# Optimization experiments

Measured on AMD Instinct MI355X. Metric: run time of the kernel, lower is better.

The kernel has to match this reference:

```python
import jax, jax.numpy as jnp
import numpy as np
from jax import lax

L, H, DH, D, FF = 8, 16, 64, 1024, 4096  # layers, heads, head dim, model dim, mlp hidden
B, S = 4, 512
EPS = 1e-5


def setup_inputs() -> dict:
    key = jax.random.key(0)
    ks = jax.random.split(key, 8)
    std = 0.02
    return {
        "x": jax.random.normal(ks[0], (B, S, D), jnp.float32),
        "ln1_w": jnp.ones((L, D), jnp.float32),
        "ln1_b": jnp.zeros((L, D), jnp.float32),
        "qw": jax.random.normal(ks[1], (L, H, DH, DH), jnp.float32) * std,
        "qb": jnp.zeros((L, H, DH), jnp.float32),
        "kw": jax.random.normal(ks[2], (L, H, DH, DH), jnp.float32) * std,
        "kb": jnp.zeros((L, H, DH), jnp.float32),
        "vw": jax.random.normal(ks[3], (L, H, DH, DH), jnp.float32) * std,
        "vb": jnp.zeros((L, H, DH), jnp.float32),
        "ln2_w": jnp.ones((L, D), jnp.float32),
        "ln2_b": jnp.zeros((L, D), jnp.float32),
        "w1": jax.random.normal(ks[4], (L, D, FF), jnp.float32) * std,
        "b1": jnp.zeros((L, FF), jnp.float32),
        "w2": jax.random.normal(ks[5], (L, FF, D), jnp.float32) * std,
        "b2": jnp.zeros((L, D), jnp.float32),
    }


def _layernorm(x, w, b):
    m = jnp.mean(x, axis=-1, keepdims=True)
    v = jnp.mean(jnp.square(x - m), axis=-1, keepdims=True)
    return (x - m) * lax.rsqrt(v + EPS) * w + b


def reference(x, ln1_w, ln1_b, qw, qb, kw, kb, vw, vb, ln2_w, ln2_b, w1, b1, w2, b2):
    b, s, d = x.shape
    scale = 1.0 / jnp.sqrt(jnp.asarray(DH, x.dtype))

    def layer(h, p):
        (l1w, l1b, Qw, Qb, Kw, Kb, Vw, Vb, l2w, l2b, W1, B1, W2, B2) = p
        y = _layernorm(h, l1w, l1b)
        yh = y.reshape(b, s, H, DH)
        # nn.Linear per head: y @ W.T + b, W is [out=e, in=d]
        q = jnp.einsum('bshd,hed->bshe', yh, Qw) + Qb
        k = jnp.einsum('bshd,hed->bshe', yh, Kw) + Kb
        v = jnp.einsum('bshd,hed->bshe', yh, Vw) + Vb
        attn = jax.nn.softmax(jnp.einsum('bshe,bthe->bhst', q, k) * scale, axis=-1)
        o = jnp.einsum('bhst,bthe->bshe', attn, v).reshape(b, s, d)
        h = h + o
        z = _layernorm(h, l2w, l2b)
        z = jax.nn.gelu(z @ W1 + B1, approximate=False) @ W2 + B2
        return h + z, None

    params = (ln1_w, ln1_b, qw, qb, kw, kb, vw, vb, ln2_w, ln2_b, w1, b1, w2, b2)
    out, _ = lax.scan(layer, x, params)
    return out
```

## Files before the change

kernel.cpp:

```cpp
#include <hip/hip_runtime.h>
#include <hip/hip_bf16.h>

typedef __hip_bfloat16 bf16;
typedef __bf16 bf16x8 __attribute__((ext_vector_type(8)));
typedef float f32x4 __attribute__((ext_vector_type(4)));
typedef unsigned short u16;
typedef unsigned int u32;

#define SEQ 512
#define DMODEL 1024
#define FFDIM 4096
#define NHEAD 16
#define HDIM 64
#define NB 4
#define NLAYER 8

#define SBAR() asm volatile("s_barrier" ::: "memory")

__device__ __forceinline__ u16 f2bu(float f) {
    union { bf16 h; u16 u; } c; c.h = __float2bfloat16(f); return c.u;
}

__device__ __forceinline__ void gload16(const bf16* g, bf16* l) {
    __builtin_amdgcn_global_load_lds(
        (const __attribute__((address_space(1))) unsigned int*)g,
        (__attribute__((address_space(3))) unsigned int*)l,
        16, 0, 0);
}

__device__ __forceinline__ void gemm_pipe(
    const bf16* __restrict__ A, int lda,
    const bf16* __restrict__ B, int ldb,
    int nkt,
    f32x4 (&acc)[8][2],
    char* lA, char* lB)
{
    const int tid = threadIdx.x;
    const int lane = tid & 63;
    const int wave = tid >> 6;
    const int wr = wave >> 2, wc = wave & 3;
    const int l15 = lane & 15, l4 = lane >> 4;

    auto stage = [&](int c, int t) {
        const bf16* Ak = A + t * 64;
        const bf16* Bk = B + t * 64;
        bf16* dA = (bf16*)(lA + c * 32768);
        bf16* dB = (bf16*)(lB + c * 16384);
#pragma unroll
        for (int it = 0; it < 4; ++it) {
            const int e = (it * 512 + tid) * 8;
            const int r = e >> 6;
            const int cb = (e & 63) * 2;
            const int sc = (cb ^ (((r >> 2) & 1) << 5)) >> 1;
            gload16(Ak + (long)r * lda + sc, dA + e);
        }
#pragma unroll
        for (int it = 0; it < 2; ++it) {
            const int e = (it * 512 + tid) * 8;
            const int r = e >> 6;
            const int cb = (e & 63) * 2;
            const int sc = (cb ^ (((r >> 2) & 1) << 5)) >> 1;
            gload16(Bk + (long)r * ldb + sc, dB + e);
        }
    };

    stage(0, 0);
    stage(1, 1);
    asm volatile("s_waitcnt vmcnt(6)" ::: "memory");
    SBAR();

    for (int t = 0; t < nkt; ++t) {
        const int cur = t & 1;
        const char* bA = lA + cur * 32768;
        const char* bB = lB + cur * 16384;

        bf16x8 bf_[2][2];
#pragma unroll
        for (int fn = 0; fn < 2; ++fn)
#pragma unroll
            for (int ks = 0; ks < 2; ++ks) {
                const int row = wc * 32 + fn * 16 + l15;
                int byte = row * 128 + (ks * 32 + l4 * 8) * 2;
                byte ^= ((row >> 2) & 1) << 5;
                bf_[fn][ks] = *(const bf16x8*)(bB + byte);
            }
#pragma unroll
        for (int q = 0; q < 4; ++q) {
            bf16x8 af[2][2];
#pragma unroll
            for (int i = 0; i < 2; ++i)
#pragma unroll
                for (int ks = 0; ks < 2; ++ks) {
                    const int row = wr * 128 + (q * 2 + i) * 16 + l15;
                    int byte = row * 128 + (ks * 32 + l4 * 8) * 2;
                    byte ^= ((row >> 2) & 1) << 5;
                    af[i][ks] = *(const bf16x8*)(bA + byte);
                }
            __builtin_amdgcn_s_setprio(1);
#pragma unroll
            for (int i = 0; i < 2; ++i)
#pragma unroll
                for (int fn = 0; fn < 2; ++fn)
#pragma unroll
                    for (int ks = 0; ks < 2; ++ks)
                        acc[q * 2 + i][fn] = __builtin_amdgcn_mfma_f32_16x16x32_bf16(
                            af[i][ks], bf_[fn][ks], acc[q * 2 + i][fn], 0, 0, 0);
            __builtin_amdgcn_s_setprio(0);
        }
        SBAR();
        if (t + 2 < nkt) {
            stage(cur, t + 2);
            asm volatile("s_waitcnt vmcnt(6)" ::: "memory");
        } else {
            asm volatile("s_waitcnt vmcnt(0)" ::: "memory");
        }
        SBAR();
    }
}

__global__ __launch_bounds__(256) void k_ln(const float* __restrict__ h,
                                            const float* __restrict__ w,
                                            const float* __restrict__ bp,
                                            bf16* __restrict__ out)
{
    const int row = blockIdx.x;
    const int tid = threadIdx.x;
    const float4 x = ((const float4*)(h + (long)row * DMODEL))[tid];
    float s  = x.x + x.y + x.z + x.w;
    float s2 = x.x * x.x + x.y * x.y + x.z * x.z + x.w * x.w;
#pragma unroll
    for (int off = 32; off; off >>= 1) { s += __shfl_xor(s, off); s2 += __shfl_xor(s2, off); }
    __shared__ float rs[4], rs2[4];
    const int wave = tid >> 6;
    if ((tid & 63) == 0) { rs[wave] = s; rs2[wave] = s2; }
    __syncthreads();
    const float S1 = rs[0] + rs[1] + rs[2] + rs[3];
    const float S2 = rs2[0] + rs2[1] + rs2[2] + rs2[3];
    const float mean = S1 * (1.0f / DMODEL);
    const float var  = S2 * (1.0f / DMODEL) - mean * mean;
    const float rstd = rsqrtf(var + 1e-5f);
    const float4 wv = ((const float4*)w)[tid];
    const float4 bv = ((const float4*)bp)[tid];
    uint2 o;
    o.x = (u32)f2bu((x.x - mean) * rstd * wv.x + bv.x) |
          ((u32)f2bu((x.y - mean) * rstd * wv.y + bv.y) << 16);
    o.y = (u32)f2bu((x.z - mean) * rstd * wv.z + bv.z) |
          ((u32)f2bu((x.w - mean) * rstd * wv.w + bv.w) << 16);
    ((uint2*)(out + (long)row * DMODEL))[tid] = o;
}

__global__ __launch_bounds__(256) void k_transw_all(const float* __restrict__ w1,
                                                    const float* __restrict__ w2,
                                                    bf16* __restrict__ w1t,
                                                    bf16* __restrict__ w2t)
{
    __shared__ float t[64][65];
    int bid = blockIdx.x;
    const int l = bid >> 11;
    bid &= 2047;
    const long lofs = (long)l * DMODEL * FFDIM;
    const float* src; bf16* dst; int R, C, rb, cb;
    if (bid < 1024) {
        src = w1 + lofs; dst = w1t + lofs; R = DMODEL; C = FFDIM;
        rb = (bid >> 6) << 6; cb = (bid & 63) << 6;
    } else {
        bid -= 1024;
        src = w2 + lofs; dst = w2t + lofs; R = FFDIM; C = DMODEL;
        rb = (bid >> 4) << 6; cb = (bid & 15) << 6;
    }
    const int tid = threadIdx.x;
    const int lr = tid >> 4;
    const int lc = (tid & 15) * 4;
#pragma unroll
    for (int i = 0; i < 4; ++i) {
        const int r = i * 16 + lr;
        const float4 v = *(const float4*)(src + (long)(rb + r) * C + cb + lc);
        t[r][lc] = v.x; t[r][lc + 1] = v.y; t[r][lc + 2] = v.z; t[r][lc + 3] = v.w;
    }
    __syncthreads();
#pragma unroll
    for (int i = 0; i < 4; ++i) {
        const int c = i * 16 + lr;
        uint2 o;
        o.x = (u32)f2bu(t[lc][c])     | ((u32)f2bu(t[lc + 1][c]) << 16);
        o.y = (u32)f2bu(t[lc + 2][c]) | ((u32)f2bu(t[lc + 3][c]) << 16);
        *(uint2*)(dst + (long)(cb + c) * R + rb + lc) = o;
    }
}

__global__ __launch_bounds__(256) void k_qkv2(const bf16* __restrict__ y,
                                              const float* __restrict__ qwl,
                                              const float* __restrict__ kwl,
                                              const float* __restrict__ vwl,
                                              const float* __restrict__ qb,
                                              const float* __restrict__ kb,
                                              const float* __restrict__ vb,
                                              bf16* __restrict__ qh,
                                              bf16* __restrict__ kh,
                                              bf16* __restrict__ vt)
{
    __shared__ __align__(16) char lmem[128 * 64 * 2 + 64 * 64 * 2];
    bf16* lA = (bf16*)lmem;
    char* lBb = lmem + 128 * 64 * 2;

    const int tid = threadIdx.x;
    const int lane = tid & 63, wave = tid >> 6;
    const int l15 = lane & 15, l4 = lane >> 4;
    const int z = blockIdx.y;
    const int b = z >> 4, hd = z & 15;
    const bf16* A = y + (long)b * SEQ * DMODEL + hd * HDIM + (long)blockIdx.x * 128 * DMODEL;

#pragma unroll
    for (int it = 0; it < 4; ++it) {
        const int f = (it * 256 + tid) * 8;
        const int r = f >> 6, c = f & 63;
        gload16(A + (long)r * DMODEL + c, lA + f);
    }
    __syncthreads();

    bf16x8 qa[2][2];
#pragma unroll
    for (int fm = 0; fm < 2; ++fm)
#pragma unroll
        for (int ks = 0; ks < 2; ++ks)
            qa[fm][ks] = *(const bf16x8*)(lA + (wave * 32 + fm * 16 + l15) * 64 + ks * 32 + l4 * 8);

    for (int t = 0; t < 3; ++t) {
        __syncthreads();
        const float* Bsrc = ((t == 0) ? qwl : (t == 1) ? kwl : vwl) + (long)hd * HDIM * HDIM;
#pragma unroll
        for (int it = 0; it < 4; ++it) {
            const int f = (it * 256 + tid) * 4;
            const float4 v = *(const float4*)(Bsrc + f);
            uint2 o;
            o.x = (u32)f2bu(v.x) | ((u32)f2bu(v.y) << 16);
            o.y = (u32)f2bu(v.z) | ((u32)f2bu(v.w) << 16);
            const int row = f >> 6;
            const int byte = (f << 1) ^ ((row & 7) << 4);
            *(uint2*)(lBb + byte) = o;
        }
        __syncthreads();

        bf16x8 bfr[4][2];
#pragma unroll
        for (int fn = 0; fn < 4; ++fn)
#pragma unroll
            for (int ks = 0; ks < 2; ++ks) {
                const int row = fn * 16 + l15;
                int byte = (row << 7) + ((ks * 32 + l4 * 8) << 1);
                byte ^= (row & 7) << 4;
                bfr[fn][ks] = *(const bf16x8*)(lBb + byte);
            }
        f32x4 acc[2][4] = {};
#pragma unroll
        for (int ks = 0; ks < 2; ++ks)
#pragma unroll
            for (int fm = 0; fm < 2; ++fm)
#pragma unroll
                for (int fn = 0; fn < 4; ++fn)
                    acc[fm][fn] = __builtin_amdgcn_mfma_f32_16x16x32_bf16(
                        qa[fm][ks], bfr[fn][ks], acc[fm][fn], 0, 0, 0);

        const float* bias = (t == 0) ? qb : (t == 1) ? kb : vb;
#pragma unroll
        for (int fm = 0; fm < 2; ++fm)
#pragma unroll
            for (int fn = 0; fn < 4; ++fn)
#pragma unroll
                for (int r = 0; r < 4; ++r) {
                    const int srow = blockIdx.x * 128 + wave * 32 + fm * 16 + l4 * 4 + r;
                    const int e = fn * 16 + l15;
                    float v = acc[fm][fn][r] + bias[hd * HDIM + e];
                    if (t == 0) {
                        qh[((long)z * SEQ + srow) * HDIM + e] = __float2bfloat16(v * 0.125f);
                    } else if (t == 1) {
                        kh[((long)z * SEQ + srow) * HDIM + e] = __float2bfloat16(v);
                    } else {
                        vt[((long)z * HDIM + e) * SEQ + srow] = __float2bfloat16(v);
                    }
                }
    }
}

__global__ __launch_bounds__(256) void k_flash(const bf16* __restrict__ qh,
                                               const bf16* __restrict__ kh,
                                               const bf16* __restrict__ vt,
                                               float* __restrict__ h)
{
    __shared__ __align__(16) char lmem[24576];
    bf16* lQ = (bf16*)lmem;
    char* lKb = lmem + 8192;
    char* lVb = lmem + 16384;

    const int tid = threadIdx.x;
    const int lane = tid & 63, wave = tid >> 6;
    const int l15 = lane & 15, l4 = lane >> 4;
    const int z = blockIdx.y;
    const int b = z >> 4, hd = z & 15;
    const int q0 = blockIdx.x * 64;

    const bf16* Qsrc = qh + ((long)z * SEQ + q0) * HDIM;
#pragma unroll
    for (int it = 0; it < 2; ++it) {
        const int f = (it * 256 + tid) * 8;
        gload16(Qsrc + f, lQ + f);
    }
    __syncthreads();

    bf16x8 qa[2];
#pragma unroll
    for (int ks = 0; ks < 2; ++ks)
        qa[ks] = *(const bf16x8*)(lQ + (wave * 16 + l15) * 64 + ks * 32 + l4 * 8);

    char* lPb = lmem + wave * 2048;

    const bf16* Kbase = kh + (long)z * SEQ * HDIM;
    const bf16* Vbase = vt + (long)z * HDIM * SEQ;

    f32x4 O[4] = {};
    float mrun[4], lrun[4];
#pragma unroll
    for (int r = 0; r < 4; ++r) { mrun[r] = -1e30f; lrun[r] = 0.0f; }

    uint4 kreg[2], vreg[2];
#pragma unroll
    for (int it = 0; it < 2; ++it) {
        const int f = (it * 256 + tid) * 8;
        kreg[it] = *(const uint4*)(Kbase + f);
        const int r = f >> 6, c = f & 63;
        vreg[it] = *(const uint4*)(Vbase + (long)r * SEQ + c);
    }

    for (int kv = 0; kv < SEQ / 64; ++kv) {
        __syncthreads();
#pragma unroll
        for (int it = 0; it < 2; ++it) {
            const int f = (it * 256 + tid) * 8;
            const int r = f >> 6;
            *(uint4*)(lKb + ((f << 1) ^ ((r & 7) << 4))) = kreg[it];
            *(uint4*)(lVb + ((f << 1) ^ ((r & 7) << 4))) = vreg[it];
        }
        if (kv + 1 < SEQ / 64) {
            const bf16* Ksrc = Kbase + (kv + 1) * 64 * HDIM;
            const bf16* Vsrc = Vbase + (kv + 1) * 64;
#pragma unroll
            for (int it = 0; it < 2; ++it) {
                const int f = (it * 256 + tid) * 8;
                kreg[it] = *(const uint4*)(Ksrc + f);
                const int r = f >> 6, c = f & 63;
                vreg[it] = *(const uint4*)(Vsrc + (long)r * SEQ + c);
            }
        }
        __syncthreads();

        f32x4 sa[4];
#pragma unroll
        for (int fn = 0; fn < 4; ++fn) sa[fn] = (f32x4){0.f, 0.f, 0.f, 0.f};
#pragma unroll
        for (int ks = 0; ks < 2; ++ks)
#pragma unroll
            for (int fn = 0; fn < 4; ++fn) {
                const int row = fn * 16 + l15;
                int byte = (row << 7) + ((ks * 32 + l4 * 8) << 1);
                byte ^= (row & 7) << 4;
                const bf16x8 kb_ = *(const bf16x8*)(lKb + byte);
                sa[fn] = __builtin_amdgcn_mfma_f32_16x16x32_bf16(qa[ks], kb_, sa[fn], 0, 0, 0);
            }

#pragma unroll
        for (int r = 0; r < 4; ++r) {
            float mx = fmaxf(fmaxf(sa[0][r], sa[1][r]), fmaxf(sa[2][r], sa[3][r]));
#pragma unroll
            for (int m_ = 1; m_ < 16; m_ <<= 1) mx = fmaxf(mx, __shfl_xor(mx, m_));
            const float nm = fmaxf(mrun[r], mx);
            const float al = __expf(mrun[r] - nm);
            mrun[r] = nm;
            float p0 = __expf(sa[0][r] - nm), p1 = __expf(sa[1][r] - nm);
            float p2 = __expf(sa[2][r] - nm), p3 = __expf(sa[3][r] - nm);
            float ps = p0 + p1 + p2 + p3;
#pragma unroll
            for (int m_ = 1; m_ < 16; m_ <<= 1) ps += __shfl_xor(ps, m_);
            lrun[r] = lrun[r] * al + ps;
#pragma unroll
            for (int fn = 0; fn < 4; ++fn) O[fn][r] *= al;
            const int row = l4 * 4 + r;
            const int rsw = (row & 7) << 4;
            const int rb = row << 7;
            *(u16*)(lPb + ((rb + ((0 * 16 + l15) << 1)) ^ rsw)) = f2bu(p0);
            *(u16*)(lPb + ((rb + ((1 * 16 + l15) << 1)) ^ rsw)) = f2bu(p1);
            *(u16*)(lPb + ((rb + ((2 * 16 + l15) << 1)) ^ rsw)) = f2bu(p2);
            *(u16*)(lPb + ((rb + ((3 * 16 + l15) << 1)) ^ rsw)) = f2bu(p3);
        }

#pragma unroll
        for (int ks = 0; ks < 2; ++ks) {
            const int rowp = l15;
            int pbyte = (rowp << 7) + ((ks * 32 + l4 * 8) << 1);
            pbyte ^= (rowp & 7) << 4;
            const bf16x8 pa = *(const bf16x8*)(lPb + pbyte);
#pragma unroll
            for (int fn = 0; fn < 4; ++fn) {
                const int row = fn * 16 + l15;
                int byte = (row << 7) + ((ks * 32 + l4 * 8) << 1);
                byte ^= (row & 7) << 4;
                const bf16x8 vb_ = *(const bf16x8*)(lVb + byte);
                O[fn] = __builtin_amdgcn_mfma_f32_16x16x32_bf16(pa, vb_, O[fn], 0, 0, 0);
            }
        }
    }

    float rinv[4];
#pragma unroll
    for (int r = 0; r < 4; ++r) rinv[r] = 1.0f / lrun[r];
#pragma unroll
    for (int fn = 0; fn < 4; ++fn)
#pragma unroll
        for (int r = 0; r < 4; ++r) {
            const int srow = q0 + wave * 16 + l4 * 4 + r;
            const int e = fn * 16 + l15;
            h[((long)b * SEQ + srow) * DMODEL + hd * HDIM + e] += O[fn][r] * rinv[r];
        }
}

__global__ __launch_bounds__(512, 2) void k_gemm1(const bf16* __restrict__ zb,
                                                  const bf16* __restrict__ w1t,
                                                  const float* __restrict__ b1,
                                                  bf16* __restrict__ ff1)
{
    __shared__ __align__(16) char lmem[98304];
    const bf16* A = zb + (long)blockIdx.x * 256 * DMODEL;
    const bf16* B = w1t + (long)blockIdx.y * 128 * DMODEL;
    f32x4 acc[8][2] = {};
    gemm_pipe(A, DMODEL, B, DMODEL, DMODEL / 64, acc, lmem, lmem + 65536);

    const int lane = threadIdx.x & 63, wave = threadIdx.x >> 6;
    const int wr = wave >> 2, wc = wave & 3;
    const int l15 = lane & 15, l4 = lane >> 4;
#pragma unroll
    for (int fm = 0; fm < 8; ++fm)
#pragma unroll
        for (int fn = 0; fn < 2; ++fn)
#pragma unroll
            for (int r = 0; r < 4; ++r) {
                const int row = blockIdx.x * 256 + wr * 128 + fm * 16 + l4 * 4 + r;
                const int col = blockIdx.y * 128 + wc * 32 + fn * 16 + l15;
                const float x = acc[fm][fn][r] + b1[col];
                const float g = 0.5f * x * (1.0f + erff(x * 0.70710678118f));
                ff1[(long)row * FFDIM + col] = __float2bfloat16(g);
            }
}

__global__ __launch_bounds__(512, 2) void k_gemm2(const bf16* __restrict__ ff1,
                                                  const bf16* __restrict__ w2t,
                                                  float* __restrict__ part)
{
    __shared__ __align__(16) char lmem[98304];
    const int sk = blockIdx.z;
    const bf16* A = ff1 + (long)blockIdx.x * 256 * FFDIM + (long)sk * 1024;
    const bf16* B = w2t + (long)blockIdx.y * 128 * FFDIM + (long)sk * 1024;
    f32x4 acc[8][2] = {};
    gemm_pipe(A, FFDIM, B, FFDIM, 1024 / 64, acc, lmem, lmem + 65536);

    float* out = part + (long)sk * (NB * SEQ) * DMODEL;
    const int lane = threadIdx.x & 63, wave = threadIdx.x >> 6;
    const int wr = wave >> 2, wc = wave & 3;
    const int l15 = lane & 15, l4 = lane >> 4;
#pragma unroll
    for (int fm = 0; fm < 8; ++fm)
#pragma unroll
        for (int fn = 0; fn < 2; ++fn)
#pragma unroll
            for (int r = 0; r < 4; ++r) {
                const int row = blockIdx.x * 256 + wr * 128 + fm * 16 + l4 * 4 + r;
                const int col = blockIdx.y * 128 + wc * 32 + fn * 16 + l15;
                out[(long)row * DMODEL + col] = acc[fm][fn][r];
            }
}

__global__ __launch_bounds__(256) void k_red2ln(const float* __restrict__ part,
                                                const float* __restrict__ b2,
                                                float* __restrict__ h,
                                                const float* __restrict__ lnw,
                                                const float* __restrict__ lnb,
                                                bf16* __restrict__ y,
                                                int do_ln)
{
    constexpr long NELT = (long)NB * SEQ * DMODEL / 4;
    const long row = blockIdx.x;
    const int tid = threadIdx.x;
    const long i = row * (DMODEL / 4) + tid;
    float4 s = ((const float4*)part)[i];
    const float4 s1 = ((const float4*)part)[i + NELT];
    const float4 s2 = ((const float4*)part)[i + 2 * NELT];
    const float4 s3 = ((const float4*)part)[i + 3 * NELT];
    const float4 bv = ((const float4*)b2)[tid];
    float4 hv = ((float4*)h)[i];
    hv.x += s.x + s1.x + s2.x + s3.x + bv.x;
    hv.y += s.y + s1.y + s2.y + s3.y + bv.y;
    hv.z += s.z + s1.z + s2.z + s3.z + bv.z;
    hv.w += s.w + s1.w + s2.w + s3.w + bv.w;
    ((float4*)h)[i] = hv;

    if (!do_ln) return;
    float ss  = hv.x + hv.y + hv.z + hv.w;
    float ss2 = hv.x * hv.x + hv.y * hv.y + hv.z * hv.z + hv.w * hv.w;
#pragma unroll
    for (int off = 32; off; off >>= 1) { ss += __shfl_xor(ss, off); ss2 += __shfl_xor(ss2, off); }
    __shared__ float rs[4], rs2[4];
    const int wave = tid >> 6;
    if ((tid & 63) == 0) { rs[wave] = ss; rs2[wave] = ss2; }
    __syncthreads();
    const float S1 = rs[0] + rs[1] + rs[2] + rs[3];
    const float S2 = rs2[0] + rs2[1] + rs2[2] + rs2[3];
    const float mean = S1 * (1.0f / DMODEL);
    const float var  = S2 * (1.0f / DMODEL) - mean * mean;
    const float rstd = rsqrtf(var + 1e-5f);
    const float4 wv = ((const float4*)lnw)[tid];
    const float4 lb = ((const float4*)lnb)[tid];
    uint2 o;
    o.x = (u32)f2bu((hv.x - mean) * rstd * wv.x + lb.x) |
          ((u32)f2bu((hv.y - mean) * rstd * wv.y + lb.y) << 16);
    o.y = (u32)f2bu((hv.z - mean) * rstd * wv.z + lb.z) |
          ((u32)f2bu((hv.w - mean) * rstd * wv.w + lb.w) << 16);
    ((uint2*)(y + row * DMODEL))[tid] = o;
}

extern "C" void kernel_launch(void* const* d_in, const int* in_sizes, int n_in,
                              void* d_out, int out_size, void* d_ws, size_t ws_size,
                              hipStream_t stream)
{
    const float* x    = (const float*)d_in[0];
    const float* ln1w = (const float*)d_in[1];
    const float* ln1b = (const float*)d_in[2];
    const float* qw   = (const float*)d_in[3];
    const float* qb   = (const float*)d_in[4];
    const float* kw   = (const float*)d_in[5];
    const float* kb   = (const float*)d_in[6];
    const float* vw   = (const float*)d_in[7];
    const float* vb   = (const float*)d_in[8];
    const float* ln2w = (const float*)d_in[9];
    const float* ln2b = (const float*)d_in[10];
    const float* w1   = (const float*)d_in[11];
    const float* b1   = (const float*)d_in[12];
    const float* w2   = (const float*)d_in[13];
    const float* b2   = (const float*)d_in[14];

    char* ws = (char*)d_ws;
    const size_t MB = 1024 * 1024;
    bf16* y    = (bf16*)(ws + 0 * MB);
    bf16* zb   = (bf16*)(ws + 4 * MB);
    bf16* qh   = (bf16*)(ws + 8 * MB);
    bf16* kh   = (bf16*)(ws + 12 * MB);
    bf16* vt   = (bf16*)(ws + 16 * MB);
    bf16* ff1  = (bf16*)(ws + 20 * MB);
    float* part = (float*)(ws + 36 * MB);
    bf16* w1tA = (bf16*)(ws + 68 * MB);
    bf16* w2tA = (bf16*)(ws + 132 * MB);

    float* h = (float*)d_out;
    hipMemcpyAsync(d_out, x, (size_t)NB * SEQ * DMODEL * sizeof(float),
                   hipMemcpyDeviceToDevice, stream);

    k_transw_all<<<NLAYER * 2048, 256, 0, stream>>>(w1, w2, w1tA, w2tA);
    k_ln<<<NB * SEQ, 256, 0, stream>>>(x, ln1w, ln1b, y);

    for (int l = 0; l < NLAYER; ++l) {
        const long wofs = (long)l * DMODEL * FFDIM;
        k_qkv2<<<dim3(4, NB * NHEAD), 256, 0, stream>>>(
            y, qw + (long)l * 65536, kw + (long)l * 65536, vw + (long)l * 65536,
            qb + l * NHEAD * HDIM, kb + l * NHEAD * HDIM, vb + l * NHEAD * HDIM,
            qh, kh, vt);
        k_flash<<<dim3(SEQ / 64, NB * NHEAD), 256, 0, stream>>>(qh, kh, vt, h);
        k_ln<<<NB * SEQ, 256, 0, stream>>>(h, ln2w + l * DMODEL, ln2b + l * DMODEL, zb);
        k_gemm1<<<dim3(8, 32), 512, 0, stream>>>(zb, w1tA + wofs, b1 + l * FFDIM, ff1);
        k_gemm2<<<dim3(8, 8, 4), 512, 0, stream>>>(ff1, w2tA + wofs, part);
        const int last = (l == NLAYER - 1);
        k_red2ln<<<NB * SEQ, 256, 0, stream>>>(part, b2 + l * DMODEL, h,
                                               ln1w + (l + 1) * DMODEL * (1 - last),
                                               ln1b + (l + 1) * DMODEL * (1 - last),
                                               y, !last);
    }
}
```

Before: 1.023 ms.

## Transpose weights in registers and drop K/V register prefetch in attention

The weight transpose-and-convert kernel no longer stages a 64x64 tile through shared memory. Each thread loads a 4x4 sub-block into registers and writes the transposed bf16 values directly, which removes the LDS round trip and the barrier. The attention kernel drops its software prefetch of the next K/V tile into registers and loads each tile straight into LDS inside the loop. That lowers register pressure, possibly raising occupancy, but loses the overlap of global loads with compute.

```diff
diff --git a/kernel.cpp b/kernel.cpp
--- a/kernel.cpp
+++ b/kernel.cpp
@@ -154,7 +154,6 @@
                                                     bf16* __restrict__ w1t,
                                                     bf16* __restrict__ w2t)
 {
-    __shared__ float t[64][65];
     int bid = blockIdx.x;
     const int l = bid >> 11;
     bid &= 2047;
@@ -169,22 +168,22 @@
         rb = (bid >> 4) << 6; cb = (bid & 15) << 6;
     }
     const int tid = threadIdx.x;
-    const int lr = tid >> 4;
-    const int lc = (tid & 15) * 4;
-#pragma unroll
-    for (int i = 0; i < 4; ++i) {
-        const int r = i * 16 + lr;
-        const float4 v = *(const float4*)(src + (long)(rb + r) * C + cb + lc);
-        t[r][lc] = v.x; t[r][lc + 1] = v.y; t[r][lc + 2] = v.z; t[r][lc + 3] = v.w;
-    }
-    __syncthreads();
-#pragma unroll
-    for (int i = 0; i < 4; ++i) {
-        const int c = i * 16 + lr;
+    const int lane = tid & 63, wave = tid >> 6;
+    const int r0 = ((wave & 1) << 5) + ((lane >> 3) << 2);
+    const int c0 = ((wave >> 1) << 5) + ((lane & 7) << 2);
+
+    float4 v[4];
+#pragma unroll
+    for (int i = 0; i < 4; ++i)
+        v[i] = *(const float4*)(src + (long)(rb + r0 + i) * C + cb + c0);
+#pragma unroll
+    for (int j = 0; j < 4; ++j) {
+        const float a0 = (&v[0].x)[j], a1 = (&v[1].x)[j];
+        const float a2 = (&v[2].x)[j], a3 = (&v[3].x)[j];
         uint2 o;
-        o.x = (u32)f2bu(t[lc][c])     | ((u32)f2bu(t[lc + 1][c]) << 16);
-        o.y = (u32)f2bu(t[lc + 2][c]) | ((u32)f2bu(t[lc + 3][c]) << 16);
-        *(uint2*)(dst + (long)(cb + c) * R + rb + lc) = o;
+        o.x = (u32)f2bu(a0) | ((u32)f2bu(a1) << 16);
+        o.y = (u32)f2bu(a2) | ((u32)f2bu(a3) << 16);
+        *(uint2*)(dst + (long)(cb + c0 + j) * R + rb + r0) = o;
     }
 }
 
@@ -314,42 +313,28 @@
 
     char* lPb = lmem + wave * 2048;
 
-    const bf16* Kbase = kh + (long)z * SEQ * HDIM;
-    const bf16* Vbase = vt + (long)z * HDIM * SEQ;
-
     f32x4 O[4] = {};
     float mrun[4], lrun[4];
 #pragma unroll
     for (int r = 0; r < 4; ++r) { mrun[r] = -1e30f; lrun[r] = 0.0f; }
 
-    uint4 kreg[2], vreg[2];
-#pragma unroll
-    for (int it = 0; it < 2; ++it) {
-        const int f = (it * 256 + tid) * 8;
-        kreg[it] = *(const uint4*)(Kbase + f);
-        const int r = f >> 6, c = f & 63;
-        vreg[it] = *(const uint4*)(Vbase + (long)r * SEQ + c);
-    }
-
     for (int kv = 0; kv < SEQ / 64; ++kv) {
         __syncthreads();
+        const bf16* Ksrc = kh + ((long)z * SEQ + kv * 64) * HDIM;
 #pragma unroll
         for (int it = 0; it < 2; ++it) {
             const int f = (it * 256 + tid) * 8;
             const int r = f >> 6;
-            *(uint4*)(lKb + ((f << 1) ^ ((r & 7) << 4))) = kreg[it];
-            *(uint4*)(lVb + ((f << 1) ^ ((r & 7) << 4))) = vreg[it];
-        }
-        if (kv + 1 < SEQ / 64) {
-            const bf16* Ksrc = Kbase + (kv + 1) * 64 * HDIM;
-            const bf16* Vsrc = Vbase + (kv + 1) * 64;
-#pragma unroll
-            for (int it = 0; it < 2; ++it) {
-                const int f = (it * 256 + tid) * 8;
-                kreg[it] = *(const uint4*)(Ksrc + f);
-                const int r = f >> 6, c = f & 63;
-                vreg[it] = *(const uint4*)(Vsrc + (long)r * SEQ + c);
-            }
+            const uint4 v = *(const uint4*)(Ksrc + f);
+            *(uint4*)(lKb + ((f << 1) ^ ((r & 7) << 4))) = v;
+        }
+        const bf16* Vsrc = vt + (long)z * HDIM * SEQ + kv * 64;
+#pragma unroll
+        for (int it = 0; it < 2; ++it) {
+            const int f = (it * 256 + tid) * 8;
+            const int r = f >> 6, c = f & 63;
+            const uint4 v = *(const uint4*)(Vsrc + (long)r * SEQ + c);
+            *(uint4*)(lVb + ((f << 1) ^ ((r & 7) << 4))) = v;
         }
         __syncthreads();
 
```

Result: faster. 952.0 us (-6.9%).
